# Kernel tuning notes

Hardware: AMD Instinct MI355X
Metric: run time of the kernel (lower is better)

The kernel has to match this reference:

```python
import jax, jax.numpy as jnp
import numpy as np

N_UNITS, HASH, BASIS = 32, 1024, 128
C, H, W = 3, 64, 64
D = C * H * W  # 12288
B = 16
DEPTH = 16


def setup_inputs() -> dict:
    key = jax.random.key(0)
    k0, k1, k2, k3, k4 = jax.random.split(key, 5)
    x = jax.random.normal(k0, (B, C, H, W), dtype=jnp.float32)
    P = jax.random.normal(k1, (D, HASH), dtype=jnp.float32) / np.float32(np.sqrt(D))
    basis = jax.random.normal(k2, (N_UNITS, HASH, BASIS), dtype=jnp.float32) / np.float32(np.sqrt(HASH))
    Wt = jax.random.normal(k3, (D, D), dtype=jnp.float32) / np.float32(np.sqrt(D))
    b = jax.random.normal(k4, (N_UNITS, D), dtype=jnp.float32) * 0.01
    return {"x": x, "P": P, "basis": basis, "Wt": Wt, "b": b, "depth": DEPTH}


def reference(x, P, basis, Wt, b, depth):
    """HRN routing, inference mode (all units populated).

    Returns (hashes (B, hash_feat), routes (B, depth) int32).
    """
    Bn = x.shape[0]
    n_units, hash_feat, _ = basis.shape
    xf_all = x.reshape(Bn, -1)  # (B, D)

    def one_exemplar(xf0):
        h0 = xf0 @ P  # (HASH,) hash of the exemplar
        mask0 = jnp.ones((n_units,), dtype=bool)  # units still available
        out0 = jnp.zeros((hash_feat,), dtype=xf0.dtype)

        def step(carry, _):
            xf, h, mask, out = carry
            # projection of h onto every unit's basis: (h @ B_u) @ B_u^T
            coeff = jnp.einsum('f,ufk->uk', h, basis)
            proj = jnp.einsum('uk,ufk->uf', coeff, basis)  # (n_units, HASH)
            mags = jnp.sqrt(jnp.sum(proj * proj, axis=-1))
            mags = jnp.where(mask, mags, -jnp.inf)
            idx = jnp.argmax(mags)  # routed unit
            residual = h - proj[idx]
            out = out + residual
            mask = mask.at[idx].set(False)
            # selected unit transforms the exemplar and re-hashes
            xf2 = jnp.tanh(xf @ Wt + b[idx])
            h2 = xf2 @ P
            return (xf2, h2, mask, out), idx.astype(jnp.int32)

        (_, _, _, out), route = jax.lax.scan(step, (xf0, h0, mask0, out0), None, length=depth)
        return out, route

    hashes, routes = jax.vmap(one_exemplar)(xf_all)
    return hashes, routes
```

## Files before the change

### kernel.cpp

```cpp
#include <hip/hip_runtime.h>
#include <math.h>

#define NU     32
#define HASHF  1024
#define BASISK 128
#define DD     12288
#define BN     16
#define DEPTH  16

#define KC_Y   32
#define KCH_Y  384
#define KC_H   64
#define KCH_H  192
#define LXF_LD 12
#define CSM_LD 20

__global__ __launch_bounds__(256) void k_transpose(const float* __restrict__ x,
                                                   float* __restrict__ xfT) {
    int i = blockIdx.x * 256 + threadIdx.x;
    int b = i / DD, k = i % DD;
    xfT[(size_t)k * BN + b] = x[i];
}

__global__ __launch_bounds__(128) void k_S(const float* __restrict__ basis,
                                           float* __restrict__ S) {
    int u  = blockIdx.x >> 3;
    int it = blockIdx.x & 7;
    int t  = threadIdx.x;
    int i0 = it * 16;

    __shared__ float lrow[8 * BASISK];
    float acc[16];
#pragma unroll
    for (int i = 0; i < 16; i++) acc[i] = 0.f;

    const float* bu = basis + (size_t)u * HASHF * BASISK;
    for (int fb = 0; fb < HASHF / 8; fb++) {
#pragma unroll
        for (int r = 0; r < 8; r++)
            lrow[r * BASISK + t] = bu[(size_t)(fb * 8 + r) * BASISK + t];
        __syncthreads();
#pragma unroll
        for (int r = 0; r < 8; r++) {
            float wj = lrow[r * BASISK + t];
#pragma unroll
            for (int i = 0; i < 16; i++)
                acc[i] += lrow[r * BASISK + i0 + i] * wj;
        }
        __syncthreads();
    }
#pragma unroll
    for (int i = 0; i < 16; i++)
        S[((size_t)u * BASISK + i0 + i) * BASISK + t] = acc[i];
}

__global__ __launch_bounds__(256) void k_matP(const float* __restrict__ xfT,
                                              const float* __restrict__ P,
                                              float* __restrict__ h_part) {
    int bh = blockIdx.x & 1;
    int c  = blockIdx.x >> 1;
    int t  = threadIdx.x;
    int kbase = c * KCH_H;

    __shared__ __align__(16) float lxf[KCH_H * LXF_LD];
    for (int j = t; j < KCH_H * 8; j += 256) {
        int b_l = j & 7, fl = j >> 3;
        lxf[fl * LXF_LD + b_l] = xfT[(size_t)(kbase + fl) * BN + bh * 8 + b_l];
    }
    __syncthreads();

    int f0 = t * 4;
    float acc[8][4] = {};
    const float* wp = P + (size_t)kbase * HASHF + f0;
    for (int kl = 0; kl < KCH_H; kl++) {
        float4 w = *(const float4*)(wp + (size_t)kl * HASHF);
        const float4* xv = (const float4*)&lxf[kl * LXF_LD];
        float4 x0 = xv[0], x1 = xv[1];
        float xb[8] = {x0.x, x0.y, x0.z, x0.w, x1.x, x1.y, x1.z, x1.w};
#pragma unroll
        for (int b = 0; b < 8; b++) {
            acc[b][0] += xb[b] * w.x; acc[b][1] += xb[b] * w.y;
            acc[b][2] += xb[b] * w.z; acc[b][3] += xb[b] * w.w;
        }
    }
    float* hp = h_part + (size_t)c * (BN * HASHF) + (size_t)(bh * 8) * HASHF + f0;
#pragma unroll
    for (int b = 0; b < 8; b++)
        *(float4*)&hp[(size_t)b * HASHF] =
            make_float4(acc[b][0], acc[b][1], acc[b][2], acc[b][3]);
}

__global__ __launch_bounds__(256) void k_big(const float* __restrict__ xfT,
                                             const float* __restrict__ Wt,
                                             float* __restrict__ y_part,
                                             const float* __restrict__ h_part,
                                             const float* __restrict__ basis,
                                             float* __restrict__ coeff_part,
                                             float* __restrict__ h_full) {
    __shared__ __align__(16) float smem[KCH_Y * BN];
    int t = threadIdx.x;

    if (blockIdx.x < 128) {
        int u2 = blockIdx.x >> 3;
        int fc = blockIdx.x & 7;
        int u  = u2 * 2 + (t >> 7);
        int k  = t & 127;

        for (int j = t; j < 128 * BN; j += 256) {
            int b = j >> 7, fl = j & 127;
            float sum = 0.f;
            const float* hp = h_part + (size_t)b * HASHF + fc * 128 + fl;
#pragma unroll 4
            for (int c = 0; c < KC_H; c++) sum += hp[(size_t)c * (BN * HASHF)];
            smem[fl * CSM_LD + b] = sum;
            if (u2 == 0) h_full[(size_t)b * HASHF + fc * 128 + fl] = sum;
        }
        __syncthreads();

        float acc[BN];
#pragma unroll
        for (int b = 0; b < BN; b++) acc[b] = 0.f;
        const float* bp = basis + ((size_t)u * HASHF + fc * 128) * BASISK + k;
        for (int fl = 0; fl < 128; fl++) {
            float w = bp[(size_t)fl * BASISK];
            const float4* lv = (const float4*)&smem[fl * CSM_LD];
#pragma unroll
            for (int q = 0; q < 4; q++) {
                float4 a = lv[q];
                acc[4*q+0] += a.x * w;
                acc[4*q+1] += a.y * w;
                acc[4*q+2] += a.z * w;
                acc[4*q+3] += a.w * w;
            }
        }
#pragma unroll
        for (int b = 0; b < BN; b++)
            coeff_part[((size_t)(fc * BN + b) * NU + u) * BASISK + k] = acc[b];
    } else {
        int m  = blockIdx.x - 128;
        int nt = m % 24;
        int c  = m / 24;
        int n0 = nt * 512 + t * 2;
        int kbase = c * KCH_Y;

        for (int j = t; j < KCH_Y * BN; j += 256)
            smem[j] = xfT[(size_t)kbase * BN + j];
        __syncthreads();

        float2 acc[BN];
#pragma unroll
        for (int b = 0; b < BN; b++) acc[b] = make_float2(0.f, 0.f);

        const float* wp = Wt + (size_t)kbase * DD + n0;
        for (int kl = 0; kl < KCH_Y; kl += 8) {
            float2 w[8];
#pragma unroll
            for (int r = 0; r < 8; r++)
                w[r] = *(const float2*)(wp + (size_t)(kl + r) * DD);
#pragma unroll
            for (int r = 0; r < 8; r++) {
                const float4* xv = (const float4*)&smem[(kl + r) * BN];
#pragma unroll
                for (int q = 0; q < 4; q++) {
                    float4 a = xv[q];
                    acc[4*q+0].x += a.x * w[r].x; acc[4*q+0].y += a.x * w[r].y;
                    acc[4*q+1].x += a.y * w[r].x; acc[4*q+1].y += a.y * w[r].y;
                    acc[4*q+2].x += a.z * w[r].x; acc[4*q+2].y += a.z * w[r].y;
                    acc[4*q+3].x += a.w * w[r].x; acc[4*q+3].y += a.w * w[r].y;
                }
            }
        }
#pragma unroll
        for (int b = 0; b < BN; b++)
            *(float2*)&y_part[(size_t)c * (BN * DD) + (size_t)b * DD + n0] = acc[b];
    }
}

__global__ __launch_bounds__(128) void k_magsmax(const float* __restrict__ coeff_part,
                                                 const float* __restrict__ S,
                                                 float* __restrict__ coeff_full,
                                                 unsigned long long* __restrict__ best,
                                                 const int* __restrict__ routes, int s) {
    int b = blockIdx.x >> 5;
    int u = blockIdx.x & 31;
    int t = threadIdx.x;

    __shared__ int s_used;
    __shared__ float lc[BASISK];
    __shared__ float red[BASISK];

    if (t == 0) {
        int used = 0;
        for (int j = 0; j < s; j++) used |= (routes[b * DEPTH + j] == u);
        s_used = used;
    }
    __syncthreads();
    if (s_used) return;

    float cv = 0.f;
#pragma unroll
    for (int fc = 0; fc < 8; fc++)
        cv += coeff_part[((size_t)(fc * BN + b) * NU + u) * BASISK + t];
    lc[t] = cv;
    coeff_full[((size_t)b * NU + u) * BASISK + t] = cv;
    __syncthreads();

    float v = 0.f;
    const float* Sp = S + (size_t)u * BASISK * BASISK + t;
#pragma unroll 8
    for (int i = 0; i < BASISK; i++) v += Sp[(size_t)i * BASISK] * lc[i];

    red[t] = v * cv;
    __syncthreads();
    for (int st = 64; st > 0; st >>= 1) {
        if (t < st) red[t] += red[t + st];
        __syncthreads();
    }
    if (t == 0) {
        float mag = fmaxf(red[0], 0.f);
        unsigned long long key =
            ((unsigned long long)__float_as_uint(mag) << 6) |
            (unsigned long long)(31 - u);
        atomicMax(best + (size_t)s * BN + b, key);
    }
}

__global__ __launch_bounds__(256) void k_tail(const float* __restrict__ y_part,
                                              const float* __restrict__ bias,
                                              const unsigned long long* __restrict__ best,
                                              const float* __restrict__ P,
                                              float* __restrict__ xfT_next,
                                              float* __restrict__ h_part,
                                              const float* __restrict__ h_full,
                                              const float* __restrict__ coeff_full,
                                              const float* __restrict__ basis,
                                              float* __restrict__ out_acc,
                                              int* __restrict__ routes,
                                              int s, int nMatP) {
    int t = threadIdx.x;

    if ((int)blockIdx.x < nMatP) {
        __shared__ __align__(16) float lxf[KCH_H * LXF_LD];
        int bh = blockIdx.x & 1;
        int c  = blockIdx.x >> 1;
        int kbase = c * KCH_H;

        for (int j = t; j < KCH_H * 8; j += 256) {
            int b_l = j / KCH_H;
            int fl  = j - b_l * KCH_H;
            int b   = bh * 8 + b_l;
            float sum = 0.f;
            const float* yp = y_part + (size_t)b * DD + kbase + fl;
#pragma unroll 4
            for (int cc = 0; cc < KC_Y; cc++) sum += yp[(size_t)cc * (BN * DD)];
            int u = 31 - (int)(best[(size_t)s * BN + b] & 63ull);
            float v = tanhf(sum + bias[(size_t)u * DD + kbase + fl]);
            lxf[fl * LXF_LD + b_l] = v;
            xfT_next[(size_t)(kbase + fl) * BN + b] = v;
        }
        __syncthreads();

        int f0 = t * 4;
        float acc[8][4] = {};
        const float* wp = P + (size_t)kbase * HASHF + f0;
        for (int kl = 0; kl < KCH_H; kl++) {
            float4 w = *(const float4*)(wp + (size_t)kl * HASHF);
            const float4* xv = (const float4*)&lxf[kl * LXF_LD];
            float4 x0 = xv[0], x1 = xv[1];
            float xb[8] = {x0.x, x0.y, x0.z, x0.w, x1.x, x1.y, x1.z, x1.w};
#pragma unroll
            for (int b = 0; b < 8; b++) {
                acc[b][0] += xb[b] * w.x; acc[b][1] += xb[b] * w.y;
                acc[b][2] += xb[b] * w.z; acc[b][3] += xb[b] * w.w;
            }
        }
        float* hp = h_part + (size_t)c * (BN * HASHF) + (size_t)(bh * 8) * HASHF + f0;
#pragma unroll
        for (int b = 0; b < 8; b++)
            *(float4*)&hp[(size_t)b * HASHF] =
                make_float4(acc[b][0], acc[b][1], acc[b][2], acc[b][3]);
    } else {
        int rid = blockIdx.x - nMatP;
        int b   = rid >> 2;
        int fq  = rid & 3;
        __shared__ float lc[BASISK];

        int u = 31 - (int)(best[(size_t)s * BN + b] & 63ull);
        if (t < BASISK) lc[t] = coeff_full[((size_t)b * NU + u) * BASISK + t];
        if (t == 0 && fq == 0) routes[b * DEPTH + s] = u;
        __syncthreads();

        int f = fq * 256 + t;
        float hv = h_full[(size_t)b * HASHF + f];
        const float4* br = (const float4*)&basis[((size_t)u * HASHF + f) * BASISK];
        const float4* cr = (const float4*)lc;
        float dot = 0.f;
#pragma unroll
        for (int j = 0; j < 32; j++) {
            float4 bv = br[j], c4 = cr[j];
            dot += bv.x * c4.x + bv.y * c4.y + bv.z * c4.z + bv.w * c4.w;
        }
        out_acc[b * HASHF + f] += hv - dot;
    }
}

__global__ __launch_bounds__(256) void k_out(const float* __restrict__ out_acc,
                                             const int* __restrict__ routes,
                                             float* __restrict__ o, int n) {
    int i = blockIdx.x * 256 + threadIdx.x;
    if (i >= n) return;
    if (i < BN * HASHF) o[i] = out_acc[i];
    else o[i] = (float)routes[i - BN * HASHF];
}

extern "C" void kernel_launch(void* const* d_in, const int* in_sizes, int n_in,
                              void* d_out, int out_size, void* d_ws, size_t ws_size,
                              hipStream_t stream) {
    const float* x     = (const float*)d_in[0];
    const float* P     = (const float*)d_in[1];
    const float* basis = (const float*)d_in[2];
    const float* Wt    = (const float*)d_in[3];
    const float* bias  = (const float*)d_in[4];
    float* out = (float*)d_out;

    float* w = (float*)d_ws;
    size_t off = 0;
    auto alloc = [&](size_t nf) { float* p = w + off; off += nf; return p; };

    float* xfT0       = alloc((size_t)DD * BN);
    float* xfT1       = alloc((size_t)DD * BN);
    float* out_acc    = alloc(BN * HASHF);
    unsigned long long* best = (unsigned long long*)alloc(DEPTH * BN * 2);
    float* coeff_part = alloc((size_t)8 * BN * NU * BASISK);
    float* coeff_full = alloc((size_t)BN * NU * BASISK);
    float* h_full     = alloc((size_t)BN * HASHF);
    float* S          = alloc((size_t)NU * BASISK * BASISK);
    int*   routes     = (int*)alloc(BN * DEPTH);
    float* y_part     = alloc((size_t)KC_Y * BN * DD);
    float* h_part     = alloc((size_t)KC_H * BN * HASHF);
    (void)ws_size;

    hipMemsetAsync(out_acc, 0,
                   (size_t)BN * HASHF * sizeof(float) +
                   (size_t)DEPTH * BN * sizeof(unsigned long long), stream);

    k_transpose<<<(BN * DD) / 256, 256, 0, stream>>>(x, xfT0);
    k_S<<<NU * 8, 128, 0, stream>>>(basis, S);
    k_matP<<<2 * KC_H, 256, 0, stream>>>(xfT0, P, h_part);

    for (int s = 0; s < DEPTH; s++) {
        float* cur = (s & 1) ? xfT1 : xfT0;
        float* nxt = (s & 1) ? xfT0 : xfT1;

        int nWt = (s < DEPTH - 1) ? 24 * KC_Y : 0;
        k_big<<<128 + nWt, 256, 0, stream>>>(cur, Wt, y_part, h_part, basis,
                                             coeff_part, h_full);
        k_magsmax<<<BN * NU, 128, 0, stream>>>(coeff_part, S, coeff_full, best,
                                               routes, s);
        int nMatP = (s < DEPTH - 1) ? 2 * KC_H : 0;
        k_tail<<<nMatP + 64, 256, 0, stream>>>(y_part, bias, best, P, nxt, h_part,
                                               h_full, coeff_full, basis, out_acc,
                                               routes, s, nMatP);
    }

    k_out<<<(BN * HASHF + BN * DEPTH + 255) / 256, 256, 0, stream>>>(out_acc, routes,
                                                                     out, out_size);
}
```

Baseline: 3.795 ms.

## Widen Wt GEMV tile to float4 columns and read activations directly from global

The Wt matvec blocks now each cover 1024 output columns with float4 weight loads, which halves the number of Wt blocks. They also stop staging the xfT chunk in shared memory and read the broadcast activations straight from global (cache). The shared buffer is moved into the coeff branch only, at the smaller size that branch needs, which reduces LDS use per block. Each thread now holds 64 accumulators instead of 32, so register pressure rises, and the per-thread activation loads rely on cache hits instead of LDS.

```diff
diff --git a/kernel.cpp b/kernel.cpp
--- a/kernel.cpp
+++ b/kernel.cpp
@@ -10,6 +10,7 @@
 
 #define KC_Y   32
 #define KCH_Y  384
+#define NT_Y   12
 #define KC_H   64
 #define KCH_H  192
 #define LXF_LD 12
@@ -97,10 +98,10 @@
                                              const float* __restrict__ basis,
                                              float* __restrict__ coeff_part,
                                              float* __restrict__ h_full) {
-    __shared__ __align__(16) float smem[KCH_Y * BN];
     int t = threadIdx.x;
 
     if (blockIdx.x < 128) {
+        __shared__ __align__(16) float smem[128 * CSM_LD];
         int u2 = blockIdx.x >> 3;
         int fc = blockIdx.x & 7;
         int u  = u2 * 2 + (t >> 7);
@@ -138,41 +139,32 @@
             coeff_part[((size_t)(fc * BN + b) * NU + u) * BASISK + k] = acc[b];
     } else {
         int m  = blockIdx.x - 128;
-        int nt = m % 24;
-        int c  = m / 24;
-        int n0 = nt * 512 + t * 2;
+        int nt = m % NT_Y;
+        int c  = m / NT_Y;
+        int n0 = nt * 1024 + t * 4;
         int kbase = c * KCH_Y;
 
-        for (int j = t; j < KCH_Y * BN; j += 256)
-            smem[j] = xfT[(size_t)kbase * BN + j];
-        __syncthreads();
-
-        float2 acc[BN];
-#pragma unroll
-        for (int b = 0; b < BN; b++) acc[b] = make_float2(0.f, 0.f);
+        float4 acc[BN];
+#pragma unroll
+        for (int b = 0; b < BN; b++) acc[b] = make_float4(0.f, 0.f, 0.f, 0.f);
 
         const float* wp = Wt + (size_t)kbase * DD + n0;
-        for (int kl = 0; kl < KCH_Y; kl += 8) {
-            float2 w[8];
-#pragma unroll
-            for (int r = 0; r < 8; r++)
-                w[r] = *(const float2*)(wp + (size_t)(kl + r) * DD);
-#pragma unroll
-            for (int r = 0; r < 8; r++) {
-                const float4* xv = (const float4*)&smem[(kl + r) * BN];
-#pragma unroll
-                for (int q = 0; q < 4; q++) {
-                    float4 a = xv[q];
-                    acc[4*q+0].x += a.x * w[r].x; acc[4*q+0].y += a.x * w[r].y;
-                    acc[4*q+1].x += a.y * w[r].x; acc[4*q+1].y += a.y * w[r].y;
-                    acc[4*q+2].x += a.z * w[r].x; acc[4*q+2].y += a.z * w[r].y;
-                    acc[4*q+3].x += a.w * w[r].x; acc[4*q+3].y += a.w * w[r].y;
-                }
+        const float* xr = xfT + (size_t)kbase * BN;
+#pragma unroll 4
+        for (int kl = 0; kl < KCH_Y; kl++) {
+            float4 w = *(const float4*)(wp + (size_t)kl * DD);
+            const float* xk = xr + kl * BN;
+#pragma unroll
+            for (int b = 0; b < BN; b++) {
+                float xv = xk[b];
+                acc[b].x += xv * w.x; acc[b].y += xv * w.y;
+                acc[b].z += xv * w.z; acc[b].w += xv * w.w;
             }
         }
+        float* yp = y_part + (size_t)c * (BN * DD) + n0;
 #pragma unroll
         for (int b = 0; b < BN; b++)
-            *(float2*)&y_part[(size_t)c * (BN * DD) + (size_t)b * DD + n0] = acc[b];
+            *(float4*)&yp[(size_t)b * DD] = acc[b];
     }
 }
 
@@ -352,7 +344,7 @@
         float* cur = (s & 1) ? xfT1 : xfT0;
         float* nxt = (s & 1) ? xfT0 : xfT1;
 
-        int nWt = (s < DEPTH - 1) ? 24 * KC_Y : 0;
+        int nWt = (s < DEPTH - 1) ? KC_Y * NT_Y : 0;
         k_big<<<128 + nWt, 256, 0, stream>>>(cur, Wt, y_part, h_part, basis,
                                              coeff_part, h_full);
         k_magsmax<<<BN * NU, 128, 0, stream>>>(coeff_part, S, coeff_full, best,
```

Measured after the change: 4.301 ms. 1.13x slower.
